# Performance work log

Measured on AMD Instinct MI355X. Metric: run time of the kernel, lower is better.

Reference implementation:

```python
import jax, jax.numpy as jnp
import numpy as np

IN_C, OUT_C, K, STRIDE, PAD = 16, 32, 3, 1, 1


def setup_inputs() -> dict:
    key = jax.random.key(0)
    kx, kw = jax.random.split(key)
    x = jax.random.normal(kx, (2, IN_C, 8, 8, 32, 32), dtype=jnp.float32)
    # matches torch.randn init of nn.Parameter
    weight = jax.random.normal(kw, (OUT_C, IN_C, K, K, K, K), dtype=jnp.float32)
    bias = jnp.zeros((OUT_C,), dtype=jnp.float32)
    return {"x": x, "weight": weight, "bias": bias}


def _conv4d(x, weight):
    # 4 spatial dims; layout N C T D H W, weight O I kT kD kH kW.
    dn = jax.lax.ConvDimensionNumbers(
        lhs_spec=(0, 1, 2, 3, 4, 5),
        rhs_spec=(0, 1, 2, 3, 4, 5),
        out_spec=(0, 1, 2, 3, 4, 5),
    )
    return jax.lax.conv_general_dilated(
        x, weight,
        window_strides=(STRIDE,) * 4,
        padding=((PAD, PAD),) * 4,
        dimension_numbers=dn,
    )


def reference(x, weight, bias):
    # Same math as unfold(im2col) + matmul + bias in the torch module,
    # expressed as a single N-D convolution (implicit GEMM).
    out = _conv4d(x, weight)  # [B, out_c, oT, oD, oH, oW]
    return out + bias[None, :, None, None, None, None]
```

## Files before the change

### kernel.cpp

```cpp
#include <hip/hip_runtime.h>

#define IN_C  16
#define OUT_C 32
#define NB 2
#define TT 8
#define DD 8
#define HH 32
#define WW 32
#define TP 10
#define DP 10
#define HP 34
#define WPAD 34

#define XT_ROW_B  1088
#define XT_ELEMS  (NB*TP*DP*HP*2*WPAD*8)
#define WT_TAPS_P 84
#define WT_ELEMS  (WT_TAPS_P*2*OUT_C*8)

#define A_SLAB_B 20480
#define B_LDS_B  86016

typedef __bf16 bf16x8 __attribute__((ext_vector_type(8)));
typedef float  f32x4  __attribute__((ext_vector_type(4)));
typedef float  f32x16 __attribute__((ext_vector_type(16)));

__device__ __forceinline__ unsigned short f2bf(float f) {
    unsigned int u = __builtin_bit_cast(unsigned int, f);
    u += 0x7fffu + ((u >> 16) & 1u);
    return (unsigned short)(u >> 16);
}

__device__ __forceinline__ void gload16(const void* g, void* l) {
    __builtin_amdgcn_global_load_lds(
        (const __attribute__((address_space(1))) unsigned int*)g,
        (__attribute__((address_space(3))) unsigned int*)l, 16, 0, 0);
}

__global__ __launch_bounds__(256) void prep_kernel(const float* __restrict__ x,
                                                   const float* __restrict__ wsrc,
                                                   unsigned short* __restrict__ xt,
                                                   unsigned short* __restrict__ wt) {
    int b = blockIdx.x;
    int tid = threadIdx.x;
    if (b < 4096) {
        __shared__ unsigned short ls[WW * IN_C];
        int h = b & 31, d = (b >> 5) & 7, t = (b >> 8) & 7, n = b >> 11;
        int c = tid >> 5, w = tid & 31;
        float v0 = x[((((size_t)(n * IN_C + c)     * TT + t) * DD + d) * HH + h) * WW + w];
        float v1 = x[((((size_t)(n * IN_C + c + 8) * TT + t) * DD + d) * HH + h) * WW + w];
        ls[w * 16 + c]     = f2bf(v0);
        ls[w * 16 + c + 8] = f2bf(v1);
        __syncthreads();
        if (tid < 68) {
            int blk = tid / 34, wl = tid % 34;
            unsigned char* row = (unsigned char*)xt +
                (size_t)(((n * TP + t + 1) * DP + d + 1) * HP + h + 1) * XT_ROW_B;
            f32x4 val = {0.f, 0.f, 0.f, 0.f};
            if (wl != 0 && wl != 33)
                val = *(const f32x4*)((const unsigned char*)ls + (wl - 1) * 32 + blk * 16);
            *(f32x4*)(row + tid * 16) = val;
        }
    } else if (b < 6800) {
        int j = b - 4096;
        int n, tp, dp, hp;
        if (j < 1360)      { n = j / 680;  int r = j % 680;  tp = (r / 340) * 9; int r2 = r % 340; dp = r2 / 34;       hp = r2 % 34; }
        else if (j < 2448) { int j2 = j - 1360; n = j2 / 544; int r = j2 % 544; tp = 1 + r / 68;  int r3 = r % 68;  dp = (r3 / 34) * 9; hp = r3 % 34; }
        else               { int j3 = j - 2448; n = j3 / 128; int r = j3 % 128; tp = 1 + r / 16;  int r4 = r % 16;  dp = 1 + r4 / 2;   hp = (r4 & 1) * 33; }
        if (tid < 68) {
            unsigned char* row = (unsigned char*)xt +
                (size_t)(((n * TP + tp) * DP + dp) * HP + hp) * XT_ROW_B;
            f32x4 z = {0.f, 0.f, 0.f, 0.f};
            *(f32x4*)(row + tid * 16) = z;
        }
    } else {
        int idx = (b - 6800) * 256 + tid;
        int tap = idx >> 9;
        int r = idx & 511;
        int icblk = r >> 8, oc = (r >> 3) & 31, i8 = r & 7;
        int ic = icblk * 8 + i8;
        float v = (tap < 81) ? wsrc[(oc * IN_C + ic) * 81 + tap] : 0.0f;
        wt[idx] = f2bf(v);
    }
}

__global__ __launch_bounds__(512, 1) void conv_main_kernel(const unsigned short* __restrict__ xt,
                                                           const unsigned short* __restrict__ wt,
                                                           const float* __restrict__ bias,
                                                           float* __restrict__ out) {
    __shared__ __align__(16) unsigned char As0[A_SLAB_B];
    __shared__ __align__(16) unsigned char As1[A_SLAB_B];
    __shared__ __align__(16) unsigned char Bs[B_LDS_B];

    int bid = blockIdx.x;
    int lb  = (bid & 7) * 32 + (bid >> 3);
    int hb = lb & 1, d = (lb >> 1) & 7, t = (lb >> 4) & 7, n = lb >> 7;
    int h0 = hb * 16;
    int tid  = threadIdx.x;
    int wv   = tid >> 6;
    int lane = tid & 63;
    int l31  = lane & 31;
    int kblk = lane >> 5;

    int ab = kblk * 544 + l31 * 16;
    int bb = kblk * 512 + l31 * 16;

#pragma unroll
    for (int i = 0; i < 10; ++i)
        gload16((const unsigned char*)wt + (tid + i * 512) * 16, Bs + (tid + i * 512) * 16);
    if (tid < 256)
        gload16((const unsigned char*)wt + (tid + 5120) * 16, Bs + (tid + 5120) * 16);
    {
        const unsigned char* src = (const unsigned char*)xt +
            (size_t)(((n * TP + t) * DP + d) * HP + h0) * XT_ROW_B;
        gload16(src + tid * 16,          As0 + tid * 16);
        gload16(src + (tid + 512) * 16,  As0 + (tid + 512) * 16);
        if (tid < 256)
            gload16(src + (tid + 1024) * 16, As0 + (tid + 1024) * 16);
    }
    asm volatile("s_waitcnt vmcnt(0)" ::: "memory");
    __syncthreads();

    f32x16 acc[4];
#pragma unroll
    for (int m = 0; m < 4; ++m) acc[m] = {};

#pragma unroll
    for (int p = 0; p < 9; ++p) {
        if (wv >= 4) {
            if (p < 8) {
                const int ktn = (p + 1) / 3, kdn = (p + 1) % 3;
                const unsigned char* src = (const unsigned char*)xt +
                    (size_t)(((n * TP + t + ktn) * DP + d + kdn) * HP + h0) * XT_ROW_B;
                unsigned char* dst = (p & 1) ? As0 : As1;
                int tid2 = tid - 256;
#pragma unroll
                for (int i = 0; i < 5; ++i)
                    gload16(src + (tid2 + i * 256) * 16, dst + (tid2 + i * 256) * 16);
                asm volatile("s_waitcnt vmcnt(0)" ::: "memory");
            }
        } else {
            const unsigned char* A = (p & 1) ? As1 : As0;
            const int kt = p / 3, kd = p % 3;

            bf16x8 bf[3][3];
#pragma unroll
            for (int kh = 0; kh < 3; ++kh)
#pragma unroll
                for (int kw = 0; kw < 3; ++kw)
                    bf[kh][kw] = *(const bf16x8*)(Bs + ((kt * 27 + kd * 9 + kh * 3 + kw) << 10) + bb);

#pragma unroll
            for (int r = 0; r < 6; ++r) {
#pragma unroll
                for (int kw = 0; kw < 3; ++kw) {
                    bf16x8 a = *(const bf16x8*)(A + (4 * wv + r) * 1088 + ab + kw * 16);
#pragma unroll
                    for (int kh = 0; kh < 3; ++kh) {
                        const int m = r - kh;
                        if (m >= 0 && m < 4)
                            acc[m] = __builtin_amdgcn_mfma_f32_32x32x16_bf16(a, bf[kh][kw], acc[m], 0, 0, 0);
                    }
                }
            }
        }
        __syncthreads();
    }

    if (wv < 4) {
        float bsv = bias[l31];
#pragma unroll
        for (int m = 0; m < 4; ++m) {
            int oh = h0 + 4 * wv + m;
            float* obase = out + (((((size_t)n * OUT_C + l31) * TT + t) * DD + d) * HH + oh) * WW;
#pragma unroll
            for (int q = 0; q < 4; ++q) {
                f32x4 v = { acc[m][4 * q + 0] + bsv, acc[m][4 * q + 1] + bsv,
                            acc[m][4 * q + 2] + bsv, acc[m][4 * q + 3] + bsv };
                *(f32x4*)(obase + 8 * q + 4 * kblk) = v;
            }
        }
    }
}

extern "C" void kernel_launch(void* const* d_in, const int* in_sizes, int n_in,
                              void* d_out, int out_size, void* d_ws, size_t ws_size,
                              hipStream_t stream) {
    const float* x    = (const float*)d_in[0];
    const float* wsrc = (const float*)d_in[1];
    const float* bias = (const float*)d_in[2];
    float* out        = (float*)d_out;

    unsigned short* xt = (unsigned short*)d_ws;
    unsigned short* wt = xt + XT_ELEMS;

    prep_kernel<<<4096 + 2704 + 164, 256, 0, stream>>>(x, wsrc, xt, wt);
    conv_main_kernel<<<NB * TT * DD * 2, 512, 0, stream>>>(xt, wt, bias, out);
}
```

Measured before the change: 27.49 us.

## Halve conv block tile and stream weights per kt to fit two blocks per CU

Splits each output slab into 8-row H tiles with 256-thread blocks (2 compute, 2 loader waves) and doubles the grid. The full weight tensor is no longer resident in LDS. It is streamed per kt into two double-buffered chunks by the loader waves, cutting LDS so two blocks fit per CU. This aims to fill more CUs and overlap more latency. The cost is a larger halo overhead per output row and more weight reloads per block.

```diff
diff --git a/kernel.cpp b/kernel.cpp
--- a/kernel.cpp
+++ b/kernel.cpp
@@ -17,8 +17,8 @@
 #define WT_TAPS_P 84
 #define WT_ELEMS  (WT_TAPS_P*2*OUT_C*8)
 
-#define A_SLAB_B 20480
-#define B_LDS_B  86016
+#define A_SLAB_B 12288
+#define B_CHUNK_B 28672
 
 typedef __bf16 bf16x8 __attribute__((ext_vector_type(8)));
 typedef float  f32x4  __attribute__((ext_vector_type(4)));
@@ -83,18 +83,19 @@
     }
 }
 
-__global__ __launch_bounds__(512, 1) void conv_main_kernel(const unsigned short* __restrict__ xt,
+__global__ __launch_bounds__(256, 2) void conv_main_kernel(const unsigned short* __restrict__ xt,
                                                            const unsigned short* __restrict__ wt,
                                                            const float* __restrict__ bias,
                                                            float* __restrict__ out) {
     __shared__ __align__(16) unsigned char As0[A_SLAB_B];
     __shared__ __align__(16) unsigned char As1[A_SLAB_B];
-    __shared__ __align__(16) unsigned char Bs[B_LDS_B];
+    __shared__ __align__(16) unsigned char Bs0[B_CHUNK_B];
+    __shared__ __align__(16) unsigned char Bs1[B_CHUNK_B];
 
     int bid = blockIdx.x;
-    int lb  = (bid & 7) * 32 + (bid >> 3);
-    int hb = lb & 1, d = (lb >> 1) & 7, t = (lb >> 4) & 7, n = lb >> 7;
-    int h0 = hb * 16;
+    int lb  = (bid & 7) * 64 + (bid >> 3);
+    int hb = lb & 3, d = (lb >> 2) & 7, t = (lb >> 5) & 7, n = lb >> 8;
+    int h0 = hb * 8;
     int tid  = threadIdx.x;
     int wv   = tid >> 6;
     int lane = tid & 63;
@@ -105,17 +106,14 @@
     int bb = kblk * 512 + l31 * 16;
 
 #pragma unroll
-    for (int i = 0; i < 10; ++i)
-        gload16((const unsigned char*)wt + (tid + i * 512) * 16, Bs + (tid + i * 512) * 16);
-    if (tid < 256)
-        gload16((const unsigned char*)wt + (tid + 5120) * 16, Bs + (tid + 5120) * 16);
+    for (int i = 0; i < 7; ++i)
+        gload16((const unsigned char*)wt + (tid + i * 256) * 16, Bs0 + (tid + i * 256) * 16);
     {
         const unsigned char* src = (const unsigned char*)xt +
             (size_t)(((n * TP + t) * DP + d) * HP + h0) * XT_ROW_B;
-        gload16(src + tid * 16,          As0 + tid * 16);
-        gload16(src + (tid + 512) * 16,  As0 + (tid + 512) * 16);
-        if (tid < 256)
-            gload16(src + (tid + 1024) * 16, As0 + (tid + 1024) * 16);
+#pragma unroll
+        for (int i = 0; i < 3; ++i)
+            gload16(src + (tid + i * 256) * 16, As0 + (tid + i * 256) * 16);
     }
     asm volatile("s_waitcnt vmcnt(0)" ::: "memory");
     __syncthreads();
@@ -126,28 +124,39 @@
 
 #pragma unroll
     for (int p = 0; p < 9; ++p) {
-        if (wv >= 4) {
+        const int kt = p / 3, ph3 = p % 3;
+        if (wv >= 2) {
+            int tid2 = tid - 128;
             if (p < 8) {
                 const int ktn = (p + 1) / 3, kdn = (p + 1) % 3;
                 const unsigned char* src = (const unsigned char*)xt +
                     (size_t)(((n * TP + t + ktn) * DP + d + kdn) * HP + h0) * XT_ROW_B;
-                unsigned char* dst = (p & 1) ? As0 : As1;
-                int tid2 = tid - 256;
-#pragma unroll
-                for (int i = 0; i < 5; ++i)
-                    gload16(src + (tid2 + i * 256) * 16, dst + (tid2 + i * 256) * 16);
-                asm volatile("s_waitcnt vmcnt(0)" ::: "memory");
-            }
+                unsigned char* dst = ((p + 1) & 1) ? As1 : As0;
+#pragma unroll
+                for (int i = 0; i < 6; ++i)
+                    gload16(src + (tid2 + i * 128) * 16, dst + (tid2 + i * 128) * 16);
+            }
+            if (ph3 <= 1 && kt < 2) {
+                int base = ph3 * 896;
+                const unsigned char* bsrc = (const unsigned char*)wt +
+                    (size_t)((kt + 1) * 27 * 64 + base) * 16;
+                unsigned char* bdst = (((kt + 1) & 1) ? Bs1 : Bs0) + base * 16;
+#pragma unroll
+                for (int i = 0; i < 7; ++i)
+                    gload16(bsrc + (tid2 + i * 128) * 16, bdst + (tid2 + i * 128) * 16);
+            }
+            asm volatile("s_waitcnt vmcnt(0)" ::: "memory");
         } else {
             const unsigned char* A = (p & 1) ? As1 : As0;
-            const int kt = p / 3, kd = p % 3;
+            const unsigned char* B = (kt & 1) ? Bs1 : Bs0;
+            const int kd = ph3;
 
             bf16x8 bf[3][3];
 #pragma unroll
             for (int kh = 0; kh < 3; ++kh)
 #pragma unroll
                 for (int kw = 0; kw < 3; ++kw)
-                    bf[kh][kw] = *(const bf16x8*)(Bs + ((kt * 27 + kd * 9 + kh * 3 + kw) << 10) + bb);
+                    bf[kh][kw] = *(const bf16x8*)(B + ((kd * 9 + kh * 3 + kw) << 10) + bb);
 
 #pragma unroll
             for (int r = 0; r < 6; ++r) {
@@ -166,7 +175,7 @@
         __syncthreads();
     }
 
-    if (wv < 4) {
+    if (wv < 2) {
         float bsv = bias[l31];
 #pragma unroll
         for (int m = 0; m < 4; ++m) {
@@ -194,5 +203,5 @@
     unsigned short* wt = xt + XT_ELEMS;
 
     prep_kernel<<<4096 + 2704 + 164, 256, 0, stream>>>(x, wsrc, xt, wt);
-    conv_main_kernel<<<NB * TT * DD * 2, 512, 0, stream>>>(xt, wt, bias, out);
-}
+    conv_main_kernel<<<NB * TT * DD * 4, 256, 0, stream>>>(xt, wt, bias, out);
+}
```

New measurement: 27.83 us. No clear change (+1.2%).
